# Kernel optimization log

Measured on AMD Instinct MI355X. Metric: run time of the kernel, lower is better.

The kernel has to match this reference:

```python
import jax, jax.numpy as jnp
import numpy as np

EPS = 1e-5
D_EMB = 512   # latent_codex_size
K_EMB = 1014  # codex_number


def _conv1d(x, w, stride):
    # x: (N, Cin, L), w: (Cout, Cin, K)
    return jax.lax.conv_general_dilated(
        x, w, (stride,), 'VALID', dimension_numbers=('NCH', 'OIH', 'NCH'))


def setup_inputs() -> dict:
    key = jax.random.key(0)
    ks = jax.random.split(key, 12)
    B, C, L = 2, 105, 5500
    s = 0.02  # conv weight init scale
    return {
        'input_embeddings_batch': jax.random.normal(ks[0], (B, C, L), jnp.float32),
        'input_masks_batch': jnp.zeros((B, 56), jnp.int32),
        'input_masks_invert': jnp.zeros((B, 56), jnp.int32),
        'target_ids_batch_converted': jnp.zeros((B, 56), jnp.int32),
        # wav2vec2 feature-extractor conv stack (no bias)
        'W0': jax.random.normal(ks[1], (512, 1, 10), jnp.float32) * s,
        'g0': jnp.ones((512,), jnp.float32),   # GroupNorm(512,512) gamma
        'b0': jnp.zeros((512,), jnp.float32),  # GroupNorm beta
        'W1': jax.random.normal(ks[2], (512, 512, 3), jnp.float32) * s,
        'W2': jax.random.normal(ks[3], (512, 512, 3), jnp.float32) * s,
        'W3': jax.random.normal(ks[4], (512, 512, 3), jnp.float32) * s,
        'W4': jax.random.normal(ks[5], (512, 512, 3), jnp.float32) * s,
        'W5': jax.random.normal(ks[6], (512, 512, 2), jnp.float32) * s,
        # 1x1 channel-fusion Conv2d(105 -> 1) weight + bias
        'fusion_w': jax.random.normal(ks[7], (105,), jnp.float32) * 0.1,
        'fusion_b': jnp.zeros((), jnp.float32),
        # NearestEmbed codebook, stored (K, D) (torch stores (D, K))
        'codebook': jax.random.normal(ks[8], (K_EMB, D_EMB), jnp.float32),
    }


def _encode(x, W0, g0, b0, W1, W2, W3, W4, W5, fusion_w, fusion_b):
    B, C, L = x.shape
    h = x.reshape(B * C, 1, L)
    h = _conv1d(h, W0, 3)
    # GroupNorm with 512 groups over 512 channels == per-channel norm over time
    mu = h.mean(-1, keepdims=True)
    var = h.var(-1, keepdims=True)
    h = (h - mu) * jax.lax.rsqrt(var + EPS) * g0[None, :, None] + b0[None, :, None]
    h = jax.nn.gelu(h, approximate=False)
    for w in (W1, W2, W3, W4):
        h = jax.nn.gelu(_conv1d(h, w, 2), approximate=False)
    h = jax.nn.gelu(_conv1d(h, W5, 2), approximate=False)
    D, T = h.shape[1], h.shape[2]
    f = h.reshape(B, C, D, T)
    # 1x1 conv fusing 105 channels -> 1, then squeeze
    z_e = jnp.einsum('bcdt,c->bdt', f, fusion_w) + fusion_b  # (B, D, T)
    return z_e


def _quantize(z, codebook):
    # z: (B, D, T); codebook: (K, D)
    B, D, T = z.shape
    zt = z.transpose(0, 2, 1).reshape(-1, D)  # (B*T, D)
    d = ((zt * zt).sum(-1, keepdims=True)
         - 2.0 * zt @ codebook.T
         + (codebook * codebook).sum(-1)[None, :])  # (B*T, K)
    idx = jnp.argmin(d, axis=-1)
    q = codebook[idx].reshape(B, T, D).transpose(0, 2, 1)
    return q, idx


def reference(input_embeddings_batch, input_masks_batch, input_masks_invert,
              target_ids_batch_converted, W0, g0, b0, W1, W2, W3, W4, W5,
              fusion_w, fusion_b, codebook):
    z_e = _encode(input_embeddings_batch, W0, g0, b0, W1, W2, W3, W4, W5,
                  fusion_w, fusion_b)
    z_q, _ = _quantize(z_e, codebook)           # emb(z_e, weight_sg=True)
    emb, _ = _quantize(z_e, codebook)           # emb(z_e.detach()) - same values
    return (z_q, z_e, emb)
```

## Files before the change

kernel.cpp:

```cpp
#include <hip/hip_runtime.h>
#include <math.h>


typedef __attribute__((ext_vector_type(4))) int i32x4;
typedef __attribute__((ext_vector_type(16))) int i32x16;

__device__ __forceinline__ float gelu_f(float x) {
  return 0.5f * x * (1.0f + erff(x * 0.70710678118654752440f));
}

__device__ __forceinline__ void gl_lds16(const void* g, void* l) {
  __builtin_amdgcn_global_load_lds(
      (const __attribute__((address_space(1))) void*)g,
      (__attribute__((address_space(3))) void*)l, 16, 0, 0);
}

#define S_ACT 4096.0f
#define S_W   262144.0f
#define OSCALE 9.31322574615478516e-10f

__device__ __forceinline__ int quant16(float v, float s) {
  float qf = fminf(fmaxf(rintf(v * s), -32768.f), 32639.f);
  return (int)qf;
}

__global__ __launch_bounds__(256)
void k_wprep8(const float* __restrict__ W, signed char* __restrict__ o,
              int KK, int nunits) {
  int idx = blockIdx.x * 256 + threadIdx.x;
  if (idx >= nunits) return;
  int u = idx & 7, row = (idx >> 3) & 63, rest = idx >> 9;
  int k = rest % KK, blk = rest / KK, c16 = blk & 15, ct = blk >> 4;
  int ul = u ^ (row & 7);
  int co = ct * 128 + 2 * row + (ul >> 2);
  int hl = (ul >> 1) & 1, kh = ul & 1;
  int cib = c16 * 32 + kh * 16;
  signed char* dst = o + (size_t)idx * 16;
#pragma unroll 4
  for (int j = 0; j < 16; ++j) {
    float w = W[((size_t)co * 512 + cib + j) * KK + k];
    int q = quant16(w, S_W);
    int hi = (q + 128) >> 8;
    dst[j] = (signed char)(hl ? (q - (hi << 8)) : hi);
  }
}

#define EL4(c, i) ((i) == 0 ? (c).x : (i) == 1 ? (c).y : (i) == 2 ? (c).z : (c).w)
#define AW(i) ((i) < 4 ? EL4(c0, (i)) : (i) < 8 ? EL4(c1, (i) - 4) : \
               (i) < 12 ? EL4(c2, (i) - 8) : (i) < 16 ? EL4(c3, (i) - 12) : \
               (i) < 20 ? EL4(c4, (i) - 16) : EL4(c5, (i) - 20))

__global__ __launch_bounds__(256)
void k_conv0a(const float* __restrict__ x, const float* __restrict__ w0,
              float2* __restrict__ part) {
  __shared__ __align__(16) float xl[720];
  const int n = blockIdx.y, seg = blockIdx.x, tid = threadIdx.x;
  const int s0 = seg * 232;
  const int base = 3 * s0;
  const float* xn = x + (size_t)n * 5500;
  for (int i = tid; i < 720; i += 256) {
    int gi = base + i;
    xl[i] = (gi < 5500) ? xn[gi] : 0.f;
  }
  __syncthreads();
  const int ch0 = tid, ch1 = 256 + tid;
  float wr0[10], wr1[10];
#pragma unroll
  for (int k = 0; k < 10; ++k) {
    wr0[k] = w0[ch0 * 10 + k];
    wr1[k] = w0[ch1 * 10 + k];
  }
  float sa = 0.f, sqa = 0.f, sb = 0.f, sqb = 0.f;
  for (int g = 0; g < 58; ++g) {
    const float4 c0 = *(const float4*)&xl[12 * g];
    const float4 c1 = *(const float4*)&xl[12 * g + 4];
    const float4 c2 = *(const float4*)&xl[12 * g + 8];
    const float4 c3 = *(const float4*)&xl[12 * g + 12];
    const float4 c4 = *(const float4*)&xl[12 * g + 16];
    const float4 c5 = *(const float4*)&xl[12 * g + 20];
#pragma unroll
    for (int j = 0; j < 4; ++j) {
      int t = s0 + 4 * g + j;
      if (t < 1831) {
        float h0 = 0.f, h1 = 0.f;
#pragma unroll
        for (int k = 0; k < 10; ++k) {
          float xv = AW(3 * j + k);
          h0 += wr0[k] * xv;
          h1 += wr1[k] * xv;
        }
        sa += h0; sqa += h0 * h0;
        sb += h1; sqb += h1 * h1;
      }
    }
  }
  part[((size_t)(n * 512 + ch0)) * 8 + seg] = make_float2(sa, sqa);
  part[((size_t)(n * 512 + ch1)) * 8 + seg] = make_float2(sb, sqb);
}

__global__ __launch_bounds__(256)
void k_conv0s(const float2* __restrict__ part, float2* __restrict__ stats) {
  const int n = blockIdx.x, tid = threadIdx.x;
#pragma unroll
  for (int h = 0; h < 2; ++h) {
    int ch = h * 256 + tid;
    const float2* p = part + ((size_t)(n * 512 + ch)) * 8;
    float S = 0.f, S2 = 0.f;
#pragma unroll
    for (int s = 0; s < 8; ++s) { float2 v = p[s]; S += v.x; S2 += v.y; }
    float mean = S * (1.f / 1831.f);
    float var = S2 * (1.f / 1831.f) - mean * mean;
    stats[n * 512 + ch] = make_float2(mean, rsqrtf(var + 1e-5f));
  }
}

__global__ __launch_bounds__(256)
void k_conv0b(const float* __restrict__ x, const float* __restrict__ w0,
              const float* __restrict__ g0, const float* __restrict__ b0,
              const float2* __restrict__ stats,
              signed char* __restrict__ oHi, signed char* __restrict__ oLo,
              size_t oStride) {
  __shared__ __align__(16) float xl[720];
  const int n = blockIdx.y, seg = blockIdx.x, tid = threadIdx.x;
  const int s0 = seg * 232;
  const int base = 3 * s0;
  const float* xn = x + (size_t)n * 5500;
  for (int i = tid; i < 720; i += 256) {
    int gi = base + i;
    xl[i] = (gi < 5500) ? xn[gi] : 0.f;
  }
  __syncthreads();
  const int ch0 = tid, ch1 = 256 + tid;
  float wr0[10], wr1[10];
#pragma unroll
  for (int k = 0; k < 10; ++k) {
    wr0[k] = w0[ch0 * 10 + k];
    wr1[k] = w0[ch1 * 10 + k];
  }
  const float2 st0 = stats[n * 512 + ch0];
  const float2 st1 = stats[n * 512 + ch1];
  const float sc0 = st0.y * g0[ch0], off0 = b0[ch0] - st0.x * sc0;
  const float sc1 = st1.y * g0[ch1], off1 = b0[ch1] - st1.x * sc1;
  signed char* dh = oHi + (size_t)n * oStride;
  signed char* dl = oLo + (size_t)n * oStride;
  for (int g = 0; g < 58; ++g) {
    const float4 c0 = *(const float4*)&xl[12 * g];
    const float4 c1 = *(const float4*)&xl[12 * g + 4];
    const float4 c2 = *(const float4*)&xl[12 * g + 8];
    const float4 c3 = *(const float4*)&xl[12 * g + 12];
    const float4 c4 = *(const float4*)&xl[12 * g + 16];
    const float4 c5 = *(const float4*)&xl[12 * g + 20];
#pragma unroll
    for (int j = 0; j < 4; ++j) {
      int t = s0 + 4 * g + j;
      if (t < 1831) {
        float h0 = 0.f, h1 = 0.f;
#pragma unroll
        for (int k = 0; k < 10; ++k) {
          float xv = AW(3 * j + k);
          h0 += wr0[k] * xv;
          h1 += wr1[k] * xv;
        }
        float v0 = gelu_f(h0 * sc0 + off0);
        float v1 = gelu_f(h1 * sc1 + off1);
        int q0 = quant16(v0, S_ACT), q1 = quant16(v1, S_ACT);
        int hi0 = (q0 + 128) >> 8, hi1 = (q1 + 128) >> 8;
        dh[(size_t)t * 512 + ch0] = (signed char)hi0;
        dl[(size_t)t * 512 + ch0] = (signed char)(q0 - (hi0 << 8));
        dh[(size_t)t * 512 + ch1] = (signed char)hi1;
        dl[(size_t)t * 512 + ch1] = (signed char)(q1 - (hi1 << 8));
      }
    }
  }
}

template <int KK, bool FP32OUT>
__global__ __launch_bounds__(256, 2)
void k_iconv(const signed char* __restrict__ inHi,
             const signed char* __restrict__ inLo,
             const signed char* __restrict__ wq,
             signed char* __restrict__ outHi, signed char* __restrict__ outLo,
             float* __restrict__ outF,
             int Tin, int Tout, size_t inStride, size_t outStride,
             int nt, int np) {
  const int id = blockIdx.x;
  const int pp = (id >> 5) * 8 + (id & 7);
  if (pp >= np) return;
  const int y = (id >> 3) & 3;
  const int tx = pp % nt, img = pp / nt;

  __shared__ __align__(16) signed char Asm[KK * 8192];
  __shared__ __align__(16) signed char Bsm[9216];
  const int tid = threadIdx.x;
  const int wave = tid >> 6, lane = tid & 63;
  const int lm = lane & 31, lq = lane >> 5;
  const int wco = wave & 1, wt = wave >> 1;
  const int t0 = tx * 64;
  const int co0 = y * 128;
  const size_t imgIn = (size_t)img * inStride;

  i32x16 hh[2] = {}, mm[2] = {}, ll[2] = {};

  for (int ci0 = 0; ci0 < 512; ci0 += 32) {
    __syncthreads();
    const size_t abase = ((size_t)y * 16 + (ci0 >> 5)) * (KK * 8192);
#pragma unroll
    for (int jj = 0; jj < KK * 2; ++jj) {
      int cid = (wave * KK * 2 + jj) * 64 + lane;
      gl_lds16(wq + abase + (size_t)cid * 16, Asm + cid * 16);
    }
    for (int j = wave; j < 9; j += 4) {
      int cid = j * 64 + lane;
      int row = cid >> 3, up = cid & 7;
      int ul = up ^ (row & 7);
      int pos = 2 * row + (ul >> 2);
      int hl = (ul >> 1) & 1, kh = ul & 1;
      int pg = 2 * t0 + pos;
      if (pg > Tin - 1) pg = Tin - 1;
      const signed char* src = (hl ? inLo : inHi) + imgIn +
                               (size_t)pg * 512 + ci0 + kh * 16;
      gl_lds16(src, Bsm + cid * 16);
    }
    __syncthreads();
#pragma unroll
    for (int k = 0; k < KK; ++k) {
      i32x4 ah[2], al[2];
#pragma unroll
      for (int cs = 0; cs < 2; ++cs) {
        int co_l = wco * 64 + cs * 32 + lm;
        int rowA = k * 64 + (co_l >> 1);
        int ub = (co_l & 1) * 4 + lq;
        const signed char* rp = Asm + rowA * 128;
        ah[cs] = *(const i32x4*)(rp + ((ub ^ (rowA & 7)) << 4));
        al[cs] = *(const i32x4*)(rp + (((ub + 2) ^ (rowA & 7)) << 4));
      }
      int pos = 2 * (wt * 32 + lm) + k;
      int rowB = pos >> 1;
      int vb = (pos & 1) * 4 + lq;
      const signed char* rpb = Bsm + rowB * 128;
      i32x4 bh = *(const i32x4*)(rpb + ((vb ^ (rowB & 7)) << 4));
      i32x4 bl = *(const i32x4*)(rpb + (((vb + 2) ^ (rowB & 7)) << 4));
#pragma unroll
      for (int cs = 0; cs < 2; ++cs) {
        hh[cs] = __builtin_amdgcn_mfma_i32_32x32x32_i8(ah[cs], bh, hh[cs], 0, 0, 0);
        mm[cs] = __builtin_amdgcn_mfma_i32_32x32x32_i8(ah[cs], bl, mm[cs], 0, 0, 0);
        mm[cs] = __builtin_amdgcn_mfma_i32_32x32x32_i8(al[cs], bh, mm[cs], 0, 0, 0);
        ll[cs] = __builtin_amdgcn_mfma_i32_32x32x32_i8(al[cs], bl, ll[cs], 0, 0, 0);
      }
    }
  }

  const int t = t0 + wt * 32 + lm;
  if (t < Tout) {
#pragma unroll
    for (int cs = 0; cs < 2; ++cs) {
#pragma unroll
      for (int rg = 0; rg < 4; ++rg) {
        int cbase = co0 + wco * 64 + cs * 32 + 8 * rg + 4 * lq;
        float v[4];
#pragma unroll
        for (int i = 0; i < 4; ++i) {
          int r = rg * 4 + i;
          float f = (float)hh[cs][r] * 65536.f + (float)mm[cs][r] * 256.f +
                    (float)ll[cs][r];
          v[i] = gelu_f(f * OSCALE);
        }
        if constexpr (FP32OUT) {
          *(float4*)(outF + (size_t)img * outStride +
                     (size_t)t * 512 + cbase) = make_float4(v[0], v[1], v[2], v[3]);
        } else {
          union { int w; signed char b[4]; } hv, lv;
#pragma unroll
          for (int i = 0; i < 4; ++i) {
            int q = quant16(v[i], S_ACT);
            int hi = (q + 128) >> 8;
            hv.b[i] = (signed char)hi;
            lv.b[i] = (signed char)(q - (hi << 8));
          }
          size_t o = (size_t)img * outStride + (size_t)t * 512 + cbase;
          *(int*)(outHi + o) = hv.w;
          *(int*)(outLo + o) = lv.w;
        }
      }
    }
  }
}

__global__ __launch_bounds__(256)
void k_fusion(const float* __restrict__ h5, const float* __restrict__ fw,
              const float* __restrict__ fb, float* __restrict__ ze) {
  __shared__ float fwl[105];
  const int t = blockIdx.x, b = blockIdx.y;
  const int tid = threadIdx.x;
  if (tid < 105) fwl[tid] = fw[tid];
  __syncthreads();
  const int d0 = tid * 2;
  float a0 = fb[0], a1 = fb[0];
  const float* p = h5 + ((size_t)b * 105 * 56 + t) * 512 + d0;
  for (int c = 0; c < 105; ++c) {
    float2 v = *(const float2*)(p + (size_t)c * 56 * 512);
    a0 += v.x * fwl[c];
    a1 += v.y * fwl[c];
  }
  ze[((size_t)b * 512 + d0) * 56 + t] = a0;
  ze[((size_t)b * 512 + d0 + 1) * 56 + t] = a1;
}

__global__ __launch_bounds__(256)
void k_quant(const float* __restrict__ ze, const float* __restrict__ cb,
             float* __restrict__ zq, float* __restrict__ emb) {
  __shared__ float zl[512];
  __shared__ float bw[4];
  __shared__ int bki[4];
  __shared__ int fin;
  const int t = blockIdx.x, b = blockIdx.y;
  const int tid = threadIdx.x;
  for (int d = tid; d < 512; d += 256) zl[d] = ze[((size_t)b * 512 + d) * 56 + t];
  __syncthreads();
  const int wid = tid >> 6, lane = tid & 63;
  const float4 z0 = *(const float4*)&zl[lane * 8];
  const float4 z1 = *(const float4*)&zl[lane * 8 + 4];
  float best = 3.4e38f;
  int bestk = 1 << 30;
  for (int k = wid; k < 1014; k += 4) {
    const float* cr = cb + (size_t)k * 512 + lane * 8;
    const float4 c0 = *(const float4*)cr;
    const float4 c1 = *(const float4*)(cr + 4);
    float cc = c0.x * c0.x + c0.y * c0.y + c0.z * c0.z + c0.w * c0.w
             + c1.x * c1.x + c1.y * c1.y + c1.z * c1.z + c1.w * c1.w;
    float dz = c0.x * z0.x + c0.y * z0.y + c0.z * z0.z + c0.w * z0.w
             + c1.x * z1.x + c1.y * z1.y + c1.z * z1.z + c1.w * z1.w;
    float v = cc - 2.f * dz;
#pragma unroll
    for (int o = 32; o > 0; o >>= 1) v += __shfl_xor(v, o);
    if (v < best) { best = v; bestk = k; }
  }
  if (lane == 0) { bw[wid] = best; bki[wid] = bestk; }
  __syncthreads();
  if (tid == 0) {
    float fv = bw[0];
    int fk = bki[0];
    for (int wq = 1; wq < 4; ++wq)
      if (bw[wq] < fv || (bw[wq] == fv && bki[wq] < fk)) { fv = bw[wq]; fk = bki[wq]; }
    fin = fk;
  }
  __syncthreads();
  const int fk = fin;
  for (int d = tid; d < 512; d += 256) {
    const float v = cb[(size_t)fk * 512 + d];
    const size_t o = ((size_t)b * 512 + d) * 56 + t;
    zq[o] = v;
    emb[o] = v;
  }
}

static inline int igrid(int nt, int nc) {
  int np = nt * nc;
  return ((np + 7) / 8) * 32;
}

extern "C" void kernel_launch(void* const* d_in, const int* in_sizes, int n_in,
                              void* d_out, int out_size, void* d_ws, size_t ws_size,
                              hipStream_t stream) {
  const float* x  = (const float*)d_in[0];
  const float* W0 = (const float*)d_in[4];
  const float* g0 = (const float*)d_in[5];
  const float* b0 = (const float*)d_in[6];
  const float* Wc[5] = {(const float*)d_in[7], (const float*)d_in[8],
                        (const float*)d_in[9], (const float*)d_in[10],
                        (const float*)d_in[11]};
  const float* fw = (const float*)d_in[12];
  const float* fb = (const float*)d_in[13];
  const float* cb = (const float*)d_in[14];
  float* out = (float*)d_out;

  const int KKs[5] = {3, 3, 3, 3, 2};
  char* p = (char*)d_ws;
  float* h5 = (float*)p;
  p += (size_t)210 * 56 * 512 * sizeof(float);
  signed char* wq[5];
  for (int l = 0; l < 5; ++l) {
    wq[l] = (signed char*)p;
    p += (size_t)KKs[l] * 524288;
  }
  const size_t persist = (size_t)(p - (char*)d_ws);
  const size_t sA = (size_t)1831 * 512;
  const size_t sB = (size_t)915 * 512;
  const size_t per_img = 2 * (sA + sB)
                       + 512 * 8 * sizeof(float2) + 512 * sizeof(float2);
  long ncl = (ws_size > persist) ? (long)((ws_size - persist) / per_img) : 1;
  int NC = ncl < 1 ? 1 : (ncl > 210 ? 210 : (int)ncl);
  float2* part  = (float2*)p;  p += (size_t)NC * 512 * 8 * sizeof(float2);
  float2* stats = (float2*)p;  p += (size_t)NC * 512 * sizeof(float2);
  signed char* AHi = (signed char*)p;
  signed char* ALo = AHi + (size_t)NC * sA;
  signed char* BHi = ALo + (size_t)NC * sA;
  signed char* BLo = BHi + (size_t)NC * sB;

  for (int l = 0; l < 5; ++l) {
    int nunits = KKs[l] * 32768;
    k_wprep8<<<(nunits + 255) / 256, 256, 0, stream>>>(Wc[l], wq[l], KKs[l],
                                                       nunits);
  }

  for (int n0 = 0; n0 < 210; n0 += NC) {
    const int nc = (210 - n0 < NC) ? (210 - n0) : NC;
    const float* xc = x + (size_t)n0 * 5500;
    k_conv0a<<<dim3(8, nc), 256, 0, stream>>>(xc, W0, part);
    k_conv0s<<<nc, 256, 0, stream>>>(part, stats);
    k_conv0b<<<dim3(8, nc), 256, 0, stream>>>(xc, W0, g0, b0, stats, AHi, ALo, sA);
    k_iconv<3, false><<<igrid(15, nc), 256, 0, stream>>>(
        AHi, ALo, wq[0], BHi, BLo, nullptr, 1831, 915, sA, sB, 15, 15 * nc);
    k_iconv<3, false><<<igrid(8, nc), 256, 0, stream>>>(
        BHi, BLo, wq[1], AHi, ALo, nullptr, 915, 457, sB, sA, 8, 8 * nc);
    k_iconv<3, false><<<igrid(4, nc), 256, 0, stream>>>(
        AHi, ALo, wq[2], BHi, BLo, nullptr, 457, 228, sA, sB, 4, 4 * nc);
    k_iconv<3, false><<<igrid(2, nc), 256, 0, stream>>>(
        BHi, BLo, wq[3], AHi, ALo, nullptr, 228, 113, sB, sA, 2, 2 * nc);
    k_iconv<2, true><<<igrid(1, nc), 256, 0, stream>>>(
        AHi, ALo, wq[4], nullptr, nullptr,
        h5 + (size_t)n0 * 56 * 512, 113, 56, sA, (size_t)56 * 512, 1, nc);
  }
  k_fusion<<<dim3(56, 2), 256, 0, stream>>>(h5, fw, fb, out + 57344);
  k_quant<<<dim3(56, 2), 256, 0, stream>>>(out + 57344, cb, out, out + 114688);
}
```

Measured before the change: 2.247 ms.

## Double-buffer LDS tiles in int8 conv kernel to overlap loads with MFMA

Doubles the LDS buffers for the weight (A) and activation (B) tiles in the int8 MFMA conv kernel. The next input-channel slice is now prefetched with global_load_lds while the current slice is being computed. Per-thread source and destination addresses are precomputed once and then advanced by a pointer increment, and each iteration uses one barrier instead of two. This aims to hide global-memory latency behind the matrix work. The cost is roughly double the shared-memory footprint, which may limit how many blocks fit per CU.

```diff
diff --git a/kernel.cpp b/kernel.cpp
--- a/kernel.cpp
+++ b/kernel.cpp
@@ -189,8 +189,8 @@
   const int y = (id >> 3) & 3;
   const int tx = pp % nt, img = pp / nt;
 
-  __shared__ __align__(16) signed char Asm[KK * 8192];
-  __shared__ __align__(16) signed char Bsm[9216];
+  __shared__ __align__(16) signed char Asm[2 * KK * 8192];
+  __shared__ __align__(16) signed char Bsm[2 * 9216];
   const int tid = threadIdx.x;
   const int wave = tid >> 6, lane = tid & 63;
   const int lm = lane & 31, lq = lane >> 5;
@@ -199,29 +199,58 @@
   const int co0 = y * 128;
   const size_t imgIn = (size_t)img * inStride;
 
+  const signed char* pA[KK * 2];
+  int dA[KK * 2];
+#pragma unroll
+  for (int jj = 0; jj < KK * 2; ++jj) {
+    int cid = (wave * KK * 2 + jj) * 64 + lane;
+    pA[jj] = wq + (size_t)y * 16 * (KK * 8192) + (size_t)cid * 16;
+    dA[jj] = cid * 16;
+  }
+  const signed char* pB[3];
+  int dB[3];
+  bool vB[3];
+#pragma unroll
+  for (int jj = 0; jj < 3; ++jj) {
+    int j = wave + 4 * jj;
+    vB[jj] = (j < 9);
+    int cid = vB[jj] ? (j * 64 + lane) : 0;
+    int row = cid >> 3, up = cid & 7;
+    int ul = up ^ (row & 7);
+    int pos = 2 * row + (ul >> 2);
+    int hl = (ul >> 1) & 1, kh = ul & 1;
+    int pg = 2 * t0 + pos;
+    if (pg > Tin - 1) pg = Tin - 1;
+    pB[jj] = (hl ? inLo : inHi) + imgIn + (size_t)pg * 512 + kh * 16;
+    dB[jj] = cid * 16;
+  }
+
   i32x16 hh[2] = {}, mm[2] = {}, ll[2] = {};
 
-  for (int ci0 = 0; ci0 < 512; ci0 += 32) {
+#pragma unroll
+  for (int jj = 0; jj < KK * 2; ++jj) gl_lds16(pA[jj], Asm + dA[jj]);
+#pragma unroll
+  for (int jj = 0; jj < 3; ++jj)
+    if (vB[jj]) gl_lds16(pB[jj], Bsm + dB[jj]);
+
+  for (int it = 0; it < 16; ++it) {
     __syncthreads();
-    const size_t abase = ((size_t)y * 16 + (ci0 >> 5)) * (KK * 8192);
-#pragma unroll
-    for (int jj = 0; jj < KK * 2; ++jj) {
-      int cid = (wave * KK * 2 + jj) * 64 + lane;
-      gl_lds16(wq + abase + (size_t)cid * 16, Asm + cid * 16);
+    if (it < 15) {
+      const int nb = (it + 1) & 1;
+#pragma unroll
+      for (int jj = 0; jj < KK * 2; ++jj) {
+        pA[jj] += KK * 8192;
+        gl_lds16(pA[jj], Asm + nb * (KK * 8192) + dA[jj]);
+      }
+#pragma unroll
+      for (int jj = 0; jj < 3; ++jj)
+        if (vB[jj]) {
+          pB[jj] += 32;
+          gl_lds16(pB[jj], Bsm + nb * 9216 + dB[jj]);
+        }
     }
-    for (int j = wave; j < 9; j += 4) {
-      int cid = j * 64 + lane;
-      int row = cid >> 3, up = cid & 7;
-      int ul = up ^ (row & 7);
-      int pos = 2 * row + (ul >> 2);
-      int hl = (ul >> 1) & 1, kh = ul & 1;
-      int pg = 2 * t0 + pos;
-      if (pg > Tin - 1) pg = Tin - 1;
-      const signed char* src = (hl ? inLo : inHi) + imgIn +
-                               (size_t)pg * 512 + ci0 + kh * 16;
-      gl_lds16(src, Bsm + cid * 16);
-    }
-    __syncthreads();
+    const signed char* Ab = Asm + (it & 1) * (KK * 8192);
+    const signed char* Bb = Bsm + (it & 1) * 9216;
 #pragma unroll
     for (int k = 0; k < KK; ++k) {
       i32x4 ah[2], al[2];
@@ -230,14 +259,14 @@
         int co_l = wco * 64 + cs * 32 + lm;
         int rowA = k * 64 + (co_l >> 1);
         int ub = (co_l & 1) * 4 + lq;
-        const signed char* rp = Asm + rowA * 128;
+        const signed char* rp = Ab + rowA * 128;
         ah[cs] = *(const i32x4*)(rp + ((ub ^ (rowA & 7)) << 4));
         al[cs] = *(const i32x4*)(rp + (((ub + 2) ^ (rowA & 7)) << 4));
       }
       int pos = 2 * (wt * 32 + lm) + k;
       int rowB = pos >> 1;
       int vb = (pos & 1) * 4 + lq;
-      const signed char* rpb = Bsm + rowB * 128;
+      const signed char* rpb = Bb + rowB * 128;
       i32x4 bh = *(const i32x4*)(rpb + ((vb ^ (rowB & 7)) << 4));
       i32x4 bl = *(const i32x4*)(rpb + (((vb + 2) ^ (rowB & 7)) << 4));
 #pragma unroll
```

After: 2.289 ms. About the same (+1.9%).

## Double time tile per block in int8 conv kernel and precompute load addresses

Applied to the files above, without the earlier changes.

Each block of the int8 split-precision conv kernel now covers 128 output time steps instead of 64. Every wave keeps two sets of accumulators per channel slice, so each loaded weight fragment feeds twice as many MFMAs and weight traffic per output halves. Per-thread input-gather addresses and the LDS weight pointer are now computed once, outside the channel loop. The trade-offs are more accumulator registers and LDS per block, which may lower occupancy, and fewer blocks per layer. The last stride-2 layer (Tout 56) now runs a 128-step tile that is mostly padding.

```diff
diff --git a/kernel.cpp b/kernel.cpp
--- a/kernel.cpp
+++ b/kernel.cpp
@@ -190,36 +190,47 @@
   const int tx = pp % nt, img = pp / nt;
 
   __shared__ __align__(16) signed char Asm[KK * 8192];
-  __shared__ __align__(16) signed char Bsm[9216];
+  __shared__ __align__(16) signed char Bsm[17408];
   const int tid = threadIdx.x;
   const int wave = tid >> 6, lane = tid & 63;
   const int lm = lane & 31, lq = lane >> 5;
   const int wco = wave & 1, wt = wave >> 1;
-  const int t0 = tx * 64;
+  const int t0 = tx * 128;
   const int co0 = y * 128;
   const size_t imgIn = (size_t)img * inStride;
 
-  i32x16 hh[2] = {}, mm[2] = {}, ll[2] = {};
-
-  for (int ci0 = 0; ci0 < 512; ci0 += 32) {
+  const signed char* pAw = wq + (size_t)y * 16 * (KK * 8192) +
+                           ((size_t)(wave * KK * 2) * 64 + lane) * 16;
+  const signed char* pB[5];
+  int dB[5];
+  bool vB[5];
+#pragma unroll
+  for (int jj = 0; jj < 5; ++jj) {
+    int j = wave + 4 * jj;
+    vB[jj] = (j < 17);
+    int cid = (j < 17 ? j : 0) * 64 + lane;
+    int row = cid >> 3, up = cid & 7;
+    int ul = up ^ (row & 7);
+    int pos = 2 * row + (ul >> 2);
+    int hl = (ul >> 1) & 1, kh = ul & 1;
+    int pg = 2 * t0 + pos;
+    if (pg > Tin - 1) pg = Tin - 1;
+    pB[jj] = (hl ? inLo : inHi) + imgIn + (size_t)pg * 512 + kh * 16;
+    dB[jj] = cid * 16;
+  }
+
+  i32x16 hh[2][2] = {}, mm[2][2] = {}, ll[2][2] = {};
+
+  for (int it = 0; it < 16; ++it) {
     __syncthreads();
-    const size_t abase = ((size_t)y * 16 + (ci0 >> 5)) * (KK * 8192);
-#pragma unroll
-    for (int jj = 0; jj < KK * 2; ++jj) {
-      int cid = (wave * KK * 2 + jj) * 64 + lane;
-      gl_lds16(wq + abase + (size_t)cid * 16, Asm + cid * 16);
-    }
-    for (int j = wave; j < 9; j += 4) {
-      int cid = j * 64 + lane;
-      int row = cid >> 3, up = cid & 7;
-      int ul = up ^ (row & 7);
-      int pos = 2 * row + (ul >> 2);
-      int hl = (ul >> 1) & 1, kh = ul & 1;
-      int pg = 2 * t0 + pos;
-      if (pg > Tin - 1) pg = Tin - 1;
-      const signed char* src = (hl ? inLo : inHi) + imgIn +
-                               (size_t)pg * 512 + ci0 + kh * 16;
-      gl_lds16(src, Bsm + cid * 16);
+    {
+      const signed char* pa = pAw + (size_t)it * (KK * 8192);
+#pragma unroll
+      for (int jj = 0; jj < KK * 2; ++jj)
+        gl_lds16(pa + jj * 1024, Asm + (wave * KK * 2 + jj) * 1024 + lane * 16);
+#pragma unroll
+      for (int jj = 0; jj < 5; ++jj)
+        if (vB[jj]) gl_lds16(pB[jj] + it * 32, Bsm + dB[jj]);
     }
     __syncthreads();
 #pragma unroll
@@ -234,52 +245,58 @@
         ah[cs] = *(const i32x4*)(rp + ((ub ^ (rowA & 7)) << 4));
         al[cs] = *(const i32x4*)(rp + (((ub + 2) ^ (rowA & 7)) << 4));
       }
-      int pos = 2 * (wt * 32 + lm) + k;
-      int rowB = pos >> 1;
-      int vb = (pos & 1) * 4 + lq;
-      const signed char* rpb = Bsm + rowB * 128;
-      i32x4 bh = *(const i32x4*)(rpb + ((vb ^ (rowB & 7)) << 4));
-      i32x4 bl = *(const i32x4*)(rpb + (((vb + 2) ^ (rowB & 7)) << 4));
-#pragma unroll
-      for (int cs = 0; cs < 2; ++cs) {
-        hh[cs] = __builtin_amdgcn_mfma_i32_32x32x32_i8(ah[cs], bh, hh[cs], 0, 0, 0);
-        mm[cs] = __builtin_amdgcn_mfma_i32_32x32x32_i8(ah[cs], bl, mm[cs], 0, 0, 0);
-        mm[cs] = __builtin_amdgcn_mfma_i32_32x32x32_i8(al[cs], bh, mm[cs], 0, 0, 0);
-        ll[cs] = __builtin_amdgcn_mfma_i32_32x32x32_i8(al[cs], bl, ll[cs], 0, 0, 0);
+#pragma unroll
+      for (int ts = 0; ts < 2; ++ts) {
+        int pos = 2 * (wt * 64 + ts * 32 + lm) + k;
+        int rowB = pos >> 1;
+        int vb = (pos & 1) * 4 + lq;
+        const signed char* rpb = Bsm + rowB * 128;
+        i32x4 bh = *(const i32x4*)(rpb + ((vb ^ (rowB & 7)) << 4));
+        i32x4 bl = *(const i32x4*)(rpb + (((vb + 2) ^ (rowB & 7)) << 4));
+#pragma unroll
+        for (int cs = 0; cs < 2; ++cs) {
+          hh[cs][ts] = __builtin_amdgcn_mfma_i32_32x32x32_i8(ah[cs], bh, hh[cs][ts], 0, 0, 0);
+          mm[cs][ts] = __builtin_amdgcn_mfma_i32_32x32x32_i8(ah[cs], bl, mm[cs][ts], 0, 0, 0);
+          mm[cs][ts] = __builtin_amdgcn_mfma_i32_32x32x32_i8(al[cs], bh, mm[cs][ts], 0, 0, 0);
+          ll[cs][ts] = __builtin_amdgcn_mfma_i32_32x32x32_i8(al[cs], bl, ll[cs][ts], 0, 0, 0);
+        }
       }
     }
   }
 
-  const int t = t0 + wt * 32 + lm;
-  if (t < Tout) {
-#pragma unroll
-    for (int cs = 0; cs < 2; ++cs) {
-#pragma unroll
-      for (int rg = 0; rg < 4; ++rg) {
-        int cbase = co0 + wco * 64 + cs * 32 + 8 * rg + 4 * lq;
-        float v[4];
-#pragma unroll
-        for (int i = 0; i < 4; ++i) {
-          int r = rg * 4 + i;
-          float f = (float)hh[cs][r] * 65536.f + (float)mm[cs][r] * 256.f +
-                    (float)ll[cs][r];
-          v[i] = gelu_f(f * OSCALE);
-        }
-        if constexpr (FP32OUT) {
-          *(float4*)(outF + (size_t)img * outStride +
-                     (size_t)t * 512 + cbase) = make_float4(v[0], v[1], v[2], v[3]);
-        } else {
-          union { int w; signed char b[4]; } hv, lv;
+#pragma unroll
+  for (int ts = 0; ts < 2; ++ts) {
+    const int t = t0 + wt * 64 + ts * 32 + lm;
+    if (t < Tout) {
+#pragma unroll
+      for (int cs = 0; cs < 2; ++cs) {
+#pragma unroll
+        for (int rg = 0; rg < 4; ++rg) {
+          int cbase = co0 + wco * 64 + cs * 32 + 8 * rg + 4 * lq;
+          float v[4];
 #pragma unroll
           for (int i = 0; i < 4; ++i) {
-            int q = quant16(v[i], S_ACT);
-            int hi = (q + 128) >> 8;
-            hv.b[i] = (signed char)hi;
-            lv.b[i] = (signed char)(q - (hi << 8));
+            int r = rg * 4 + i;
+            float f = (float)hh[cs][ts][r] * 65536.f +
+                      (float)mm[cs][ts][r] * 256.f + (float)ll[cs][ts][r];
+            v[i] = gelu_f(f * OSCALE);
           }
-          size_t o = (size_t)img * outStride + (size_t)t * 512 + cbase;
-          *(int*)(outHi + o) = hv.w;
-          *(int*)(outLo + o) = lv.w;
+          if constexpr (FP32OUT) {
+            *(float4*)(outF + (size_t)img * outStride +
+                       (size_t)t * 512 + cbase) = make_float4(v[0], v[1], v[2], v[3]);
+          } else {
+            union { int w; signed char b[4]; } hv, lv;
+#pragma unroll
+            for (int i = 0; i < 4; ++i) {
+              int q = quant16(v[i], S_ACT);
+              int hi = (q + 128) >> 8;
+              hv.b[i] = (signed char)hi;
+              lv.b[i] = (signed char)(q - (hi << 8));
+            }
+            size_t o = (size_t)img * outStride + (size_t)t * 512 + cbase;
+            *(int*)(outHi + o) = hv.w;
+            *(int*)(outLo + o) = lv.w;
+          }
         }
       }
     }
@@ -409,14 +426,14 @@
     k_conv0a<<<dim3(8, nc), 256, 0, stream>>>(xc, W0, part);
     k_conv0s<<<nc, 256, 0, stream>>>(part, stats);
     k_conv0b<<<dim3(8, nc), 256, 0, stream>>>(xc, W0, g0, b0, stats, AHi, ALo, sA);
-    k_iconv<3, false><<<igrid(15, nc), 256, 0, stream>>>(
-        AHi, ALo, wq[0], BHi, BLo, nullptr, 1831, 915, sA, sB, 15, 15 * nc);
     k_iconv<3, false><<<igrid(8, nc), 256, 0, stream>>>(
-        BHi, BLo, wq[1], AHi, ALo, nullptr, 915, 457, sB, sA, 8, 8 * nc);
+        AHi, ALo, wq[0], BHi, BLo, nullptr, 1831, 915, sA, sB, 8, 8 * nc);
     k_iconv<3, false><<<igrid(4, nc), 256, 0, stream>>>(
-        AHi, ALo, wq[2], BHi, BLo, nullptr, 457, 228, sA, sB, 4, 4 * nc);
+        BHi, BLo, wq[1], AHi, ALo, nullptr, 915, 457, sB, sA, 4, 4 * nc);
     k_iconv<3, false><<<igrid(2, nc), 256, 0, stream>>>(
-        BHi, BLo, wq[3], AHi, ALo, nullptr, 228, 113, sB, sA, 2, 2 * nc);
+        AHi, ALo, wq[2], BHi, BLo, nullptr, 457, 228, sA, sB, 2, 2 * nc);
+    k_iconv<3, false><<<igrid(1, nc), 256, 0, stream>>>(
+        BHi, BLo, wq[3], AHi, ALo, nullptr, 228, 113, sB, sA, 1, nc);
     k_iconv<2, true><<<igrid(1, nc), 256, 0, stream>>>(
         AHi, ALo, wq[4], nullptr, nullptr,
         h5 + (size_t)n0 * 56 * 512, 113, 56, sA, (size_t)56 * 512, 1, nc);
```

Result: slower. 2.434 ms (+8.4%).

## Replace LDS-staged int8 conv with direct register loads of MFMA fragments

Applied to the files above, without the earlier changes.

Removes the shared-memory staging and barriers from the split-int8 MFMA conv kernel. Each wave now loads its weight and activation fragments straight from global memory into registers, using a new weight prepack layout that matches the MFMA operand order per lane. This drops the LDS round trips and synchronisation, but data reuse across waves now relies on the L1/L2 caches, so global traffic may rise.

```diff
diff --git a/kernel.cpp b/kernel.cpp
--- a/kernel.cpp
+++ b/kernel.cpp
@@ -7,12 +7,6 @@
 
 __device__ __forceinline__ float gelu_f(float x) {
   return 0.5f * x * (1.0f + erff(x * 0.70710678118654752440f));
-}
-
-__device__ __forceinline__ void gl_lds16(const void* g, void* l) {
-  __builtin_amdgcn_global_load_lds(
-      (const __attribute__((address_space(1))) void*)g,
-      (__attribute__((address_space(3))) void*)l, 16, 0, 0);
 }
 
 #define S_ACT 4096.0f
@@ -29,19 +23,21 @@
               int KK, int nunits) {
   int idx = blockIdx.x * 256 + threadIdx.x;
   if (idx >= nunits) return;
-  int u = idx & 7, row = (idx >> 3) & 63, rest = idx >> 9;
-  int k = rest % KK, blk = rest / KK, c16 = blk & 15, ct = blk >> 4;
-  int ul = u ^ (row & 7);
-  int co = ct * 128 + 2 * row + (ul >> 2);
-  int hl = (ul >> 1) & 1, kh = ul & 1;
-  int cib = c16 * 32 + kh * 16;
+  int lane = idx & 63, chunk = idx >> 6;
+  int pl = chunk & 1, cs = (chunk >> 1) & 1;
+  int rest = chunk >> 2;
+  int k = rest % KK;
+  int it = (rest / KK) & 15;
+  int strip = rest / (KK * 16);
+  int co = strip * 64 + cs * 32 + (lane & 31);
+  int cib = it * 32 + (lane >> 5) * 16;
   signed char* dst = o + (size_t)idx * 16;
 #pragma unroll 4
   for (int j = 0; j < 16; ++j) {
     float w = W[((size_t)co * 512 + cib + j) * KK + k];
     int q = quant16(w, S_W);
     int hi = (q + 128) >> 8;
-    dst[j] = (signed char)(hl ? (q - (hi << 8)) : hi);
+    dst[j] = (signed char)(pl ? (q - (hi << 8)) : hi);
   }
 }
 
@@ -176,7 +172,7 @@
 
 template <int KK, bool FP32OUT>
 __global__ __launch_bounds__(256, 2)
-void k_iconv(const signed char* __restrict__ inHi,
+void k_rconv(const signed char* __restrict__ inHi,
              const signed char* __restrict__ inLo,
              const signed char* __restrict__ wq,
              signed char* __restrict__ outHi, signed char* __restrict__ outLo,
@@ -189,74 +185,57 @@
   const int y = (id >> 3) & 3;
   const int tx = pp % nt, img = pp / nt;
 
-  __shared__ __align__(16) signed char Asm[KK * 8192];
-  __shared__ __align__(16) signed char Bsm[9216];
   const int tid = threadIdx.x;
   const int wave = tid >> 6, lane = tid & 63;
   const int lm = lane & 31, lq = lane >> 5;
   const int wco = wave & 1, wt = wave >> 1;
   const int t0 = tx * 64;
-  const int co0 = y * 128;
-  const size_t imgIn = (size_t)img * inStride;
+  const int strip = y * 2 + wco;
+
+  const signed char* pA = wq + ((size_t)strip * (16 * KK * 4)) * 1024 +
+                          (size_t)lane * 16;
+  const int tl = wt * 32 + lm;
+  int pg = 2 * (t0 + tl);
+  const int pgmax = Tin - KK;
+  if (pg > pgmax) pg = pgmax;
+  const size_t bo = (size_t)img * inStride + (size_t)pg * 512 + lq * 16;
+  const signed char* pBh = inHi + bo;
+  const signed char* pBl = inLo + bo;
 
   i32x16 hh[2] = {}, mm[2] = {}, ll[2] = {};
 
-  for (int ci0 = 0; ci0 < 512; ci0 += 32) {
-    __syncthreads();
-    const size_t abase = ((size_t)y * 16 + (ci0 >> 5)) * (KK * 8192);
-#pragma unroll
-    for (int jj = 0; jj < KK * 2; ++jj) {
-      int cid = (wave * KK * 2 + jj) * 64 + lane;
-      gl_lds16(wq + abase + (size_t)cid * 16, Asm + cid * 16);
+#pragma unroll 2
+  for (int it = 0; it < 16; ++it) {
+    i32x4 bh[KK], bl[KK];
+#pragma unroll
+    for (int k = 0; k < KK; ++k) {
+      bh[k] = *(const i32x4*)(pBh + k * 512);
+      bl[k] = *(const i32x4*)(pBl + k * 512);
     }
-    for (int j = wave; j < 9; j += 4) {
-      int cid = j * 64 + lane;
-      int row = cid >> 3, up = cid & 7;
-      int ul = up ^ (row & 7);
-      int pos = 2 * row + (ul >> 2);
-      int hl = (ul >> 1) & 1, kh = ul & 1;
-      int pg = 2 * t0 + pos;
-      if (pg > Tin - 1) pg = Tin - 1;
-      const signed char* src = (hl ? inLo : inHi) + imgIn +
-                               (size_t)pg * 512 + ci0 + kh * 16;
-      gl_lds16(src, Bsm + cid * 16);
-    }
-    __syncthreads();
 #pragma unroll
     for (int k = 0; k < KK; ++k) {
-      i32x4 ah[2], al[2];
 #pragma unroll
       for (int cs = 0; cs < 2; ++cs) {
-        int co_l = wco * 64 + cs * 32 + lm;
-        int rowA = k * 64 + (co_l >> 1);
-        int ub = (co_l & 1) * 4 + lq;
-        const signed char* rp = Asm + rowA * 128;
-        ah[cs] = *(const i32x4*)(rp + ((ub ^ (rowA & 7)) << 4));
-        al[cs] = *(const i32x4*)(rp + (((ub + 2) ^ (rowA & 7)) << 4));
-      }
-      int pos = 2 * (wt * 32 + lm) + k;
-      int rowB = pos >> 1;
-      int vb = (pos & 1) * 4 + lq;
-      const signed char* rpb = Bsm + rowB * 128;
-      i32x4 bh = *(const i32x4*)(rpb + ((vb ^ (rowB & 7)) << 4));
-      i32x4 bl = *(const i32x4*)(rpb + (((vb + 2) ^ (rowB & 7)) << 4));
-#pragma unroll
-      for (int cs = 0; cs < 2; ++cs) {
-        hh[cs] = __builtin_amdgcn_mfma_i32_32x32x32_i8(ah[cs], bh, hh[cs], 0, 0, 0);
-        mm[cs] = __builtin_amdgcn_mfma_i32_32x32x32_i8(ah[cs], bl, mm[cs], 0, 0, 0);
-        mm[cs] = __builtin_amdgcn_mfma_i32_32x32x32_i8(al[cs], bh, mm[cs], 0, 0, 0);
-        ll[cs] = __builtin_amdgcn_mfma_i32_32x32x32_i8(al[cs], bl, ll[cs], 0, 0, 0);
+        i32x4 ah = *(const i32x4*)(pA + (k * 4 + cs * 2 + 0) * 1024);
+        i32x4 al = *(const i32x4*)(pA + (k * 4 + cs * 2 + 1) * 1024);
+        hh[cs] = __builtin_amdgcn_mfma_i32_32x32x32_i8(ah, bh[k], hh[cs], 0, 0, 0);
+        mm[cs] = __builtin_amdgcn_mfma_i32_32x32x32_i8(ah, bl[k], mm[cs], 0, 0, 0);
+        mm[cs] = __builtin_amdgcn_mfma_i32_32x32x32_i8(al, bh[k], mm[cs], 0, 0, 0);
+        ll[cs] = __builtin_amdgcn_mfma_i32_32x32x32_i8(al, bl[k], ll[cs], 0, 0, 0);
       }
     }
-  }
-
-  const int t = t0 + wt * 32 + lm;
+    pA += KK * 4096;
+    pBh += 32;
+    pBl += 32;
+  }
+
+  const int t = t0 + tl;
   if (t < Tout) {
 #pragma unroll
     for (int cs = 0; cs < 2; ++cs) {
 #pragma unroll
       for (int rg = 0; rg < 4; ++rg) {
-        int cbase = co0 + wco * 64 + cs * 32 + 8 * rg + 4 * lq;
+        int cbase = y * 128 + wco * 64 + cs * 32 + 8 * rg + 4 * lq;
         float v[4];
 #pragma unroll
         for (int i = 0; i < 4; ++i) {
@@ -409,15 +388,15 @@
     k_conv0a<<<dim3(8, nc), 256, 0, stream>>>(xc, W0, part);
     k_conv0s<<<nc, 256, 0, stream>>>(part, stats);
     k_conv0b<<<dim3(8, nc), 256, 0, stream>>>(xc, W0, g0, b0, stats, AHi, ALo, sA);
-    k_iconv<3, false><<<igrid(15, nc), 256, 0, stream>>>(
+    k_rconv<3, false><<<igrid(15, nc), 256, 0, stream>>>(
         AHi, ALo, wq[0], BHi, BLo, nullptr, 1831, 915, sA, sB, 15, 15 * nc);
-    k_iconv<3, false><<<igrid(8, nc), 256, 0, stream>>>(
+    k_rconv<3, false><<<igrid(8, nc), 256, 0, stream>>>(
         BHi, BLo, wq[1], AHi, ALo, nullptr, 915, 457, sB, sA, 8, 8 * nc);
-    k_iconv<3, false><<<igrid(4, nc), 256, 0, stream>>>(
+    k_rconv<3, false><<<igrid(4, nc), 256, 0, stream>>>(
         AHi, ALo, wq[2], BHi, BLo, nullptr, 457, 228, sA, sB, 4, 4 * nc);
-    k_iconv<3, false><<<igrid(2, nc), 256, 0, stream>>>(
+    k_rconv<3, false><<<igrid(2, nc), 256, 0, stream>>>(
         BHi, BLo, wq[3], AHi, ALo, nullptr, 228, 113, sB, sA, 2, 2 * nc);
-    k_iconv<2, true><<<igrid(1, nc), 256, 0, stream>>>(
+    k_rconv<2, true><<<igrid(1, nc), 256, 0, stream>>>(
         AHi, ALo, wq[4], nullptr, nullptr,
         h5 + (size_t)n0 * 56 * 512, 113, 56, sA, (size_t)56 * 512, 1, nc);
   }
```

Result: slower. 2.730 ms (+21.5%).
